# Kernel optimization log

Hardware: AMD Instinct MI355X
Metric: run time of the kernel (lower is better)

Reference implementation:

```python
import jax, jax.numpy as jnp
import numpy as np

N0, N1, N2 = 120000, 12000, 1024
E1, E2 = 300000, 10240
F_IN, H1, C1, NCLS = 602, 8, 8, 41
NEG_SLOPE = 0.2


def setup_inputs() -> dict:
    key = jax.random.key(0)
    ks = jax.random.split(key, 14)
    x = jax.random.normal(ks[0], (N0, F_IN), jnp.float32)
    edge_index1 = jnp.stack([
        jax.random.randint(ks[1], (E1,), 0, N0),
        jax.random.randint(ks[2], (E1,), 0, N1),
    ]).astype(jnp.int64)
    edge_index2 = jnp.stack([
        jax.random.randint(ks[3], (E2,), 0, N1),
        jax.random.randint(ks[4], (E2,), 0, N2),
    ]).astype(jnp.int64)
    s1 = 1.0 / np.sqrt(F_IN)
    s2 = 1.0 / np.sqrt(H1 * C1)
    W1 = jax.random.normal(ks[5], (F_IN, H1 * C1), jnp.float32) * s1
    att_src1 = jax.random.normal(ks[6], (H1, C1), jnp.float32) * s2
    att_dst1 = jax.random.normal(ks[7], (H1, C1), jnp.float32) * s2
    b1 = jnp.zeros((H1 * C1,), jnp.float32)
    W2 = jax.random.normal(ks[8], (H1 * C1, NCLS), jnp.float32) * s2
    att_src2 = jax.random.normal(ks[9], (1, NCLS), jnp.float32) * 0.1
    att_dst2 = jax.random.normal(ks[10], (1, NCLS), jnp.float32) * 0.1
    b2 = jnp.zeros((NCLS,), jnp.float32)
    return {"x": x, "edge_index1": edge_index1, "edge_index2": edge_index2,
            "size1": N1, "size2": N2,
            "W1": W1, "att_src1": att_src1, "att_dst1": att_dst1, "b1": b1,
            "W2": W2, "att_src2": att_src2, "att_dst2": att_dst2, "b2": b2}


def _seg_softmax(alpha, seg, n):
    # numerically stable softmax over edges grouped by destination node
    m = jax.lax.stop_gradient(jax.ops.segment_max(alpha, seg, num_segments=n))
    e = jnp.exp(alpha - m[seg])
    s = jax.ops.segment_sum(e, seg, num_segments=n)
    return e / (s[seg] + 1e-16)


def _gat_conv(x_src, x_dst, ei, W, a_src, a_dst, b, n_dst):
    H, C = a_src.shape
    h_src = (x_src @ W).reshape(-1, H, C)   # [N_src, H, C]
    h_dst = (x_dst @ W).reshape(-1, H, C)   # [N_dst, H, C]
    loop = jnp.arange(n_dst)
    src = jnp.concatenate([ei[0], loop])    # self-loops on dst nodes (PyG add_self_loops)
    dst = jnp.concatenate([ei[1], loop])
    a_s = (h_src * a_src).sum(-1)           # [N_src, H]
    a_d = (h_dst * a_dst).sum(-1)           # [N_dst, H]
    alpha = jax.nn.leaky_relu(a_s[src] + a_d[dst], NEG_SLOPE)  # [E, H]
    alpha = _seg_softmax(alpha, dst, n_dst)
    out = jax.ops.segment_sum(h_src[src] * alpha[:, :, None], dst, num_segments=n_dst)
    return out.reshape(n_dst, H * C) + b


def reference(x, edge_index1, edge_index2, size1, size2,
              W1, att_src1, att_dst1, b1, W2, att_src2, att_dst2, b2):
    h = _gat_conv(x, x[:size1], edge_index1, W1, att_src1, att_dst1, b1, size1)
    h = jax.nn.elu(h)
    h = _gat_conv(h, h[:size2], edge_index2, W2, att_src2, att_dst2, b2, size2)
    return jax.nn.log_softmax(h, axis=-1)
```

## Files before the change

kernel.cpp:

```cpp
#include <hip/hip_runtime.h>
#include <hip/hip_bf16.h>
#include <math.h>

typedef short bf16x8 __attribute__((ext_vector_type(8)));
typedef float f32x4 __attribute__((ext_vector_type(4)));

#define N0v 120000
#define N1v 12000
#define N2v 1024
#define F_INv 602
#define KPADv 608
#define HCv 64
#define NCLSv 41
#define NEGv 0.2f

__device__ __forceinline__ float b2f(unsigned short u) {
  return __uint_as_float(((unsigned int)u) << 16);
}
__device__ __forceinline__ unsigned short f2b(float f) {
  unsigned int u = __float_as_uint(f);
  u += 0x7fffu + ((u >> 16) & 1u);
  return (unsigned short)(u >> 16);
}
__device__ __forceinline__ unsigned int pk2(float lo, float hi) {
  __hip_bfloat162 h = __float22bfloat162_rn(make_float2(lo, hi));
  unsigned int u;
  __builtin_memcpy(&u, &h, 4);
  return u;
}
__device__ __forceinline__ float leaky(float v) {
  return v > 0.f ? v : NEGv * v;
}

__global__ void k_prep(const float* __restrict__ W1, unsigned short* __restrict__ Wt,
                       int* __restrict__ deg1, int* __restrict__ deg2) {
  int idx = blockIdx.x * 256 + threadIdx.x;
  if (idx < HCv * KPADv) {
    int n = idx / KPADv, k = idx % KPADv;
    Wt[idx] = (k < F_INv) ? f2b(W1[k * HCv + n]) : (unsigned short)0;
  }
  if (idx < N1v) deg1[idx] = 0;
  if (idx < N2v) deg2[idx] = 0;
}

__global__ __launch_bounds__(512, 4) void k_gemm1(const float* __restrict__ x,
                                                  const unsigned short* __restrict__ Wt,
                                                  unsigned short* __restrict__ H,
                                                  float* __restrict__ as1,
                                                  float* __restrict__ ad1,
                                                  const float* __restrict__ att_s,
                                                  const float* __restrict__ att_d) {
  __shared__ unsigned short Bs[64][328];
  __shared__ float sAtt[128];
  const int tid = threadIdx.x;
  const int wave = tid >> 6, lane = tid & 63;
  const int c15 = lane & 15, kseg = lane >> 4;
  const int block_row = blockIdx.x * 128;
  const int myrow = block_row + wave * 16 + c15;
  const float* rowp = x + (size_t)min(myrow, N0v - 1) * F_INv;

  if (tid < 128) sAtt[tid] = (tid < 64) ? att_s[tid] : att_d[tid - 64];

  auto stage = [&](int kofs, int nc8) {
    int chunks = 64 * nc8;
    for (int i = tid; i < chunks; i += 512) {
      int rr = i / nc8, cc = (i % nc8) * 8;
      *reinterpret_cast<uint4*>(&Bs[rr][cc]) =
          *reinterpret_cast<const uint4*>(Wt + (size_t)rr * KPADv + kofs + cc);
    }
  };

  f32x4 acc[4];
#pragma unroll
  for (int n = 0; n < 4; ++n) acc[n] = (f32x4){0.f, 0.f, 0.f, 0.f};

  float cur[8], nxt[8];
  auto loadA = [&](int kt, float (&f)[8]) {
    const int kb = kt * 32 + kseg * 8;
    const float* p = rowp + kb;
    if (kb + 8 <= F_INv) {
#pragma unroll
      for (int q = 0; q < 4; ++q) {
        float2 t = *reinterpret_cast<const float2*>(p + 2 * q);
        f[2 * q] = t.x;
        f[2 * q + 1] = t.y;
      }
    } else {
      float2 t = *reinterpret_cast<const float2*>(p);
      f[0] = t.x;
      f[1] = t.y;
#pragma unroll
      for (int q = 2; q < 8; ++q) f[q] = 0.f;
    }
  };
  auto compute = [&](int kt) {
    union {
      unsigned int u[4];
      bf16x8 v;
    } af;
#pragma unroll
    for (int q = 0; q < 4; ++q) af.u[q] = pk2(cur[2 * q], cur[2 * q + 1]);
    const int kk = (kt < 10 ? kt * 32 : kt * 32 - 320) + kseg * 8;
#pragma unroll
    for (int n = 0; n < 4; ++n) {
      bf16x8 b = *reinterpret_cast<const bf16x8*>(&Bs[n * 16 + c15][kk]);
      acc[n] = __builtin_amdgcn_mfma_f32_16x16x32_bf16(af.v, b, acc[n], 0, 0, 0);
    }
  };

  stage(0, 40);
  loadA(0, cur);
  __syncthreads();
#pragma unroll
  for (int kt = 0; kt < 10; ++kt) {
    loadA(kt + 1, nxt);
    compute(kt);
#pragma unroll
    for (int q = 0; q < 8; ++q) cur[q] = nxt[q];
  }
  __syncthreads();
  stage(320, 36);
  __syncthreads();
#pragma unroll
  for (int kt = 10; kt < 19; ++kt) {
    if (kt < 18) loadA(kt + 1, nxt);
    compute(kt);
    if (kt < 18) {
#pragma unroll
      for (int q = 0; q < 8; ++q) cur[q] = nxt[q];
    }
  }

  float attS[4], attD[4];
#pragma unroll
  for (int n = 0; n < 4; ++n) {
    attS[n] = sAtt[n * 16 + c15];
    attD[n] = sAtt[64 + n * 16 + c15];
  }
#pragma unroll
  for (int j = 0; j < 4; ++j) {
    int row = block_row + wave * 16 + kseg * 4 + j;
    bool rok = row < N0v;
#pragma unroll
    for (int n = 0; n < 4; ++n) {
      if (rok) H[(size_t)row * HCv + n * 16 + c15] = f2b(acc[n][j]);
      float ps = acc[n][j] * attS[n];
      float pd = acc[n][j] * attD[n];
      ps += __shfl_xor(ps, 1, 64);
      ps += __shfl_xor(ps, 2, 64);
      ps += __shfl_xor(ps, 4, 64);
      pd += __shfl_xor(pd, 1, 64);
      pd += __shfl_xor(pd, 2, 64);
      pd += __shfl_xor(pd, 4, 64);
      if (rok && ((c15 & 7) == 0)) {
        int hd = n * 2 + (c15 >> 3);
        as1[(size_t)row * 8 + hd] = ps;
        if (row < N1v) ad1[(size_t)row * 8 + hd] = pd;
      }
    }
  }
}

__global__ void k_count2x(const int* __restrict__ dst1, int E1, int* __restrict__ deg1,
                          const int* __restrict__ dst2, int E2, int* __restrict__ deg2) {
  int e = blockIdx.x * 256 + threadIdx.x;
  if (e < E1) atomicAdd(&deg1[dst1[e]], 1);
  if (e < E2) atomicAdd(&deg2[dst2[e]], 1);
}

template <int ELT>
__device__ __forceinline__ void scan_body(const int* __restrict__ deg, int* __restrict__ rs,
                                          int* __restrict__ cur, int n) {
  __shared__ int wsum[16];
  const int t = threadIdx.x, lane = t & 63, wid = t >> 6;
  int vals[ELT];
  int tot = 0;
#pragma unroll
  for (int e = 0; e < ELT; ++e) {
    int i = t * ELT + e;
    int v = (i < n) ? deg[i] : 0;
    vals[e] = v;
    tot += v;
  }
  int s = tot;
#pragma unroll
  for (int off = 1; off < 64; off <<= 1) {
    int u = __shfl_up(s, off, 64);
    if (lane >= off) s += u;
  }
  if (lane == 63) wsum[wid] = s;
  __syncthreads();
  if (t < 16) {
    int w = wsum[t];
#pragma unroll
    for (int off = 1; off < 16; off <<= 1) {
      int u = __shfl_up(w, off, 64);
      if (t >= off) w += u;
    }
    wsum[t] = w;
  }
  __syncthreads();
  int woff = (wid == 0) ? 0 : wsum[wid - 1];
  int run = woff + s - tot;
#pragma unroll
  for (int e = 0; e < ELT; ++e) {
    int i = t * ELT + e;
    if (i < n) {
      rs[i] = run;
      cur[i] = run;
    }
    run += vals[e];
  }
  if (t == 1023) rs[n] = run;
}

__global__ __launch_bounds__(1024) void k_scan2x(const int* __restrict__ deg1, int* __restrict__ rs1,
                                                 int* __restrict__ cur1, int n1,
                                                 const int* __restrict__ deg2, int* __restrict__ rs2,
                                                 int* __restrict__ cur2, int n2) {
  if (blockIdx.x == 0)
    scan_body<12>(deg1, rs1, cur1, n1);
  else
    scan_body<12>(deg2, rs2, cur2, n2);
}

__global__ void k_scatter2x(const int* __restrict__ src1, const int* __restrict__ dst1, int E1,
                            int* __restrict__ cur1, int* __restrict__ es1,
                            const int* __restrict__ src2, const int* __restrict__ dst2, int E2,
                            int* __restrict__ cur2, int* __restrict__ es2) {
  int e = blockIdx.x * 256 + threadIdx.x;
  if (e < E1) {
    int p = atomicAdd(&cur1[dst1[e]], 1);
    es1[p] = src1[e];
  }
  if (e < E2) {
    int p = atomicAdd(&cur2[dst2[e]], 1);
    es2[p] = src2[e];
  }
}

__global__ __launch_bounds__(256) void k_attn1f(const float* __restrict__ as1,
                                                const float* __restrict__ ad1,
                                                const int* __restrict__ rs,
                                                const int* __restrict__ esrc,
                                                const unsigned short* __restrict__ H,
                                                const float* __restrict__ b1,
                                                const float* __restrict__ W2,
                                                const float* __restrict__ avs,
                                                const float* __restrict__ avd,
                                                float* __restrict__ g,
                                                float* __restrict__ as2,
                                                float* __restrict__ ad2) {
  __shared__ float w[HCv * NCLSv];
  __shared__ float vs[NCLSv], vd[NCLSv];
  const int tid = threadIdx.x;
  for (int i = tid; i < HCv * NCLSv; i += 256) w[i] = W2[i];
  if (tid < NCLSv) {
    vs[tid] = avs[tid];
    vd[tid] = avd[tid];
  }
  __syncthreads();
  const int lane = tid & 63;
  const int d = blockIdx.x * 4 + (tid >> 6);
  if (d >= N1v) return;
  const int h = lane >> 3;
  const int beg = rs[d], end = rs[d + 1];
  const float adh = ad1[(size_t)d * 8 + h];
  const float a_self = leaky(as1[(size_t)d * 8 + h] + adh);

  float m0 = a_self, m1 = -1e30f, m2 = -1e30f, m3 = -1e30f;
  int p = beg;
  for (; p + 4 <= end; p += 4) {
    int s0 = esrc[p], s1 = esrc[p + 1], s2 = esrc[p + 2], s3 = esrc[p + 3];
    m0 = fmaxf(m0, leaky(as1[(size_t)s0 * 8 + h] + adh));
    m1 = fmaxf(m1, leaky(as1[(size_t)s1 * 8 + h] + adh));
    m2 = fmaxf(m2, leaky(as1[(size_t)s2 * 8 + h] + adh));
    m3 = fmaxf(m3, leaky(as1[(size_t)s3 * 8 + h] + adh));
  }
  for (; p < end; ++p) m1 = fmaxf(m1, leaky(as1[(size_t)esrc[p] * 8 + h] + adh));
  const float m = fmaxf(fmaxf(m0, m1), fmaxf(m2, m3));

  float ss0 = __expf(a_self - m), ss1 = 0.f, ss2 = 0.f, ss3 = 0.f;
  float ac0 = ss0 * b2f(H[(size_t)d * HCv + lane]), ac1 = 0.f, ac2 = 0.f, ac3 = 0.f;
  for (p = beg; p + 4 <= end; p += 4) {
    int s0 = esrc[p], s1 = esrc[p + 1], s2 = esrc[p + 2], s3 = esrc[p + 3];
    float e0 = __expf(leaky(as1[(size_t)s0 * 8 + h] + adh) - m);
    float e1 = __expf(leaky(as1[(size_t)s1 * 8 + h] + adh) - m);
    float e2 = __expf(leaky(as1[(size_t)s2 * 8 + h] + adh) - m);
    float e3 = __expf(leaky(as1[(size_t)s3 * 8 + h] + adh) - m);
    ac0 += e0 * b2f(H[(size_t)s0 * HCv + lane]);
    ac1 += e1 * b2f(H[(size_t)s1 * HCv + lane]);
    ac2 += e2 * b2f(H[(size_t)s2 * HCv + lane]);
    ac3 += e3 * b2f(H[(size_t)s3 * HCv + lane]);
    ss0 += e0;
    ss1 += e1;
    ss2 += e2;
    ss3 += e3;
  }
  for (; p < end; ++p) {
    int s = esrc[p];
    float e = __expf(leaky(as1[(size_t)s * 8 + h] + adh) - m);
    ss1 += e;
    ac1 += e * b2f(H[(size_t)s * HCv + lane]);
  }
  const float ssum = (ss0 + ss1) + (ss2 + ss3);
  const float acc = (ac0 + ac1) + (ac2 + ac3);
  float o = acc / ssum + b1[lane];
  o = o > 0.f ? o : expm1f(o);

  const int lc = (lane < NCLSv) ? lane : 0;
  float gc = 0.f;
#pragma unroll
  for (int k = 0; k < HCv; ++k) {
    float bc = __shfl(o, k, 64);
    gc += bc * w[k * NCLSv + lc];
  }
  if (lane < NCLSv) g[(size_t)d * NCLSv + lane] = gc;
  float sa = (lane < NCLSv) ? gc * vs[lane] : 0.f;
  float da = (lane < NCLSv) ? gc * vd[lane] : 0.f;
#pragma unroll
  for (int off = 32; off >= 1; off >>= 1) {
    sa += __shfl_xor(sa, off, 64);
    da += __shfl_xor(da, off, 64);
  }
  if (lane == 0) {
    as2[d] = sa;
    ad2[d] = da;
  }
}

__global__ __launch_bounds__(256) void k_attn2(const float* __restrict__ as2,
                                               const float* __restrict__ ad2,
                                               const int* __restrict__ rs,
                                               const int* __restrict__ esrc,
                                               const float* __restrict__ g,
                                               const float* __restrict__ b2,
                                               float* __restrict__ out) {
  int wave = threadIdx.x >> 6, lane = threadIdx.x & 63;
  int d = blockIdx.x * 4 + wave;
  if (d >= N2v) return;
  int beg = rs[d], end = rs[d + 1];
  float ad = ad2[d];
  float a_self = leaky(as2[d] + ad);
  float m = a_self;
  for (int p = beg; p < end; ++p) m = fmaxf(m, leaky(as2[esrc[p]] + ad));
  float ssum, acc;
  {
    float e = __expf(a_self - m);
    ssum = e;
    acc = (lane < NCLSv) ? e * g[(size_t)d * NCLSv + lane] : 0.f;
  }
  for (int p = beg; p < end; ++p) {
    int s = esrc[p];
    float e = __expf(leaky(as2[s] + ad) - m);
    ssum += e;
    if (lane < NCLSv) acc += e * g[(size_t)s * NCLSv + lane];
  }
  float logit = acc / ssum + ((lane < NCLSv) ? b2[lane] : 0.f);
  float v = (lane < NCLSv) ? logit : -INFINITY;
  float mx = v;
#pragma unroll
  for (int o = 32; o >= 1; o >>= 1) mx = fmaxf(mx, __shfl_xor(mx, o, 64));
  float p = (lane < NCLSv) ? __expf(v - mx) : 0.f;
  float sum = p;
#pragma unroll
  for (int o = 32; o >= 1; o >>= 1) sum += __shfl_xor(sum, o, 64);
  if (lane < NCLSv) out[(size_t)d * NCLSv + lane] = v - mx - logf(sum);
}

extern "C" void kernel_launch(void* const* d_in, const int* in_sizes, int n_in,
                              void* d_out, int out_size, void* d_ws, size_t ws_size,
                              hipStream_t stream) {
  const float* x = (const float*)d_in[0];
  const int* ei1 = (const int*)d_in[1];
  const int* ei2 = (const int*)d_in[2];
  const float* W1 = (const float*)d_in[5];
  const float* att_src1 = (const float*)d_in[6];
  const float* att_dst1 = (const float*)d_in[7];
  const float* b1 = (const float*)d_in[8];
  const float* W2 = (const float*)d_in[9];
  const float* att_src2 = (const float*)d_in[10];
  const float* att_dst2 = (const float*)d_in[11];
  const float* b2 = (const float*)d_in[12];
  float* out = (float*)d_out;

  const int E1 = in_sizes[1] / 2;
  const int E2 = in_sizes[2] / 2;
  const int* src1 = ei1;
  const int* dst1 = ei1 + E1;
  const int* src2 = ei2;
  const int* dst2 = ei2 + E2;

  char* w = (char*)d_ws;
  size_t off = 0;
  auto alloc = [&](size_t bytes) {
    void* p = w + off;
    off += (bytes + 255) & ~(size_t)255;
    return p;
  };
  unsigned short* Wt  = (unsigned short*)alloc((size_t)HCv * KPADv * 2);
  unsigned short* H   = (unsigned short*)alloc((size_t)N0v * HCv * 2);
  float* as1 = (float*)alloc((size_t)N0v * 8 * 4);
  float* ad1 = (float*)alloc((size_t)N1v * 8 * 4);
  int* deg1  = (int*)alloc((size_t)N1v * 4);
  int* rs1   = (int*)alloc((size_t)(N1v + 1) * 4);
  int* cur1  = (int*)alloc((size_t)N1v * 4);
  int* es1   = (int*)alloc((size_t)E1 * 4);
  float* g   = (float*)alloc((size_t)N1v * NCLSv * 4);
  float* as2 = (float*)alloc((size_t)N1v * 4);
  float* ad2 = (float*)alloc((size_t)N1v * 4);
  int* deg2  = (int*)alloc((size_t)N2v * 4);
  int* rs2   = (int*)alloc((size_t)(N2v + 1) * 4);
  int* cur2  = (int*)alloc((size_t)N2v * 4);
  int* es2   = (int*)alloc((size_t)E2 * 4);
  (void)ws_size; (void)n_in; (void)out_size;

  k_prep<<<(HCv * KPADv + 255) / 256, 256, 0, stream>>>(W1, Wt, deg1, deg2);
  k_gemm1<<<(N0v + 127) / 128, 512, 0, stream>>>(x, Wt, H, as1, ad1, att_src1, att_dst1);

  k_count2x<<<(E1 + 255) / 256, 256, 0, stream>>>(dst1, E1, deg1, dst2, E2, deg2);
  k_scan2x<<<2, 1024, 0, stream>>>(deg1, rs1, cur1, N1v, deg2, rs2, cur2, N2v);
  k_scatter2x<<<(E1 + 255) / 256, 256, 0, stream>>>(src1, dst1, E1, cur1, es1,
                                                    src2, dst2, E2, cur2, es2);
  k_attn1f<<<(N1v + 3) / 4, 256, 0, stream>>>(as1, ad1, rs1, es1, H, b1,
                                              W2, att_src2, att_dst2, g, as2, ad2);
  k_attn2<<<N2v / 4, 256, 0, stream>>>(as2, ad2, rs2, es2, g, b2, out);
}
```

Baseline: 186.4 us.

## Fuse degree count into GEMM and merge graph tail into a cooperative kernel

Result: slower. 455.4 us (+144.3%).

```diff
diff --git a/kernel.cpp b/kernel.cpp
--- a/kernel.cpp
+++ b/kernel.cpp
@@ -1,6 +1,9 @@
 #include <hip/hip_runtime.h>
 #include <hip/hip_bf16.h>
+#include <hip/hip_cooperative_groups.h>
 #include <math.h>
+
+namespace cg = cooperative_groups;
 
 typedef short bf16x8 __attribute__((ext_vector_type(8)));
 typedef float f32x4 __attribute__((ext_vector_type(4)));
@@ -49,7 +52,11 @@
                                                   float* __restrict__ as1,
                                                   float* __restrict__ ad1,
                                                   const float* __restrict__ att_s,
-                                                  const float* __restrict__ att_d) {
+                                                  const float* __restrict__ att_d,
+                                                  const int* __restrict__ dst1, int E1,
+                                                  int* __restrict__ deg1,
+                                                  const int* __restrict__ dst2, int E2,
+                                                  int* __restrict__ deg2) {
   __shared__ unsigned short Bs[64][328];
   __shared__ float sAtt[128];
   const int tid = threadIdx.x;
@@ -110,6 +117,11 @@
 
   stage(0, 40);
   loadA(0, cur);
+  {
+    int e = blockIdx.x * 512 + tid;
+    if (e < E1) atomicAdd(&deg1[dst1[e]], 1);
+    if (e < E2) atomicAdd(&deg2[dst2[e]], 1);
+  }
   __syncthreads();
 #pragma unroll
   for (int kt = 0; kt < 10; ++kt) {
@@ -161,67 +173,195 @@
   }
 }
 
-__global__ void k_count2x(const int* __restrict__ dst1, int E1, int* __restrict__ deg1,
-                          const int* __restrict__ dst2, int E2, int* __restrict__ deg2) {
-  int e = blockIdx.x * 256 + threadIdx.x;
-  if (e < E1) atomicAdd(&deg1[dst1[e]], 1);
-  if (e < E2) atomicAdd(&deg2[dst2[e]], 1);
-}
-
-template <int ELT>
-__device__ __forceinline__ void scan_body(const int* __restrict__ deg, int* __restrict__ rs,
-                                          int* __restrict__ cur, int n) {
-  __shared__ int wsum[16];
+__device__ void scan_seq(const int* __restrict__ deg, int* __restrict__ rs,
+                         int* __restrict__ cur, int n) {
+  __shared__ int ws[4];
   const int t = threadIdx.x, lane = t & 63, wid = t >> 6;
-  int vals[ELT];
+  const int chunk = (n + 255) >> 8;
+  const int lo = t * chunk, hi = min(n, lo + chunk);
   int tot = 0;
-#pragma unroll
-  for (int e = 0; e < ELT; ++e) {
-    int i = t * ELT + e;
-    int v = (i < n) ? deg[i] : 0;
-    vals[e] = v;
-    tot += v;
-  }
+  for (int i = lo; i < hi; ++i) tot += deg[i];
   int s = tot;
 #pragma unroll
   for (int off = 1; off < 64; off <<= 1) {
     int u = __shfl_up(s, off, 64);
     if (lane >= off) s += u;
   }
-  if (lane == 63) wsum[wid] = s;
+  if (lane == 63) ws[wid] = s;
   __syncthreads();
-  if (t < 16) {
-    int w = wsum[t];
-#pragma unroll
-    for (int off = 1; off < 16; off <<= 1) {
-      int u = __shfl_up(w, off, 64);
-      if (t >= off) w += u;
-    }
-    wsum[t] = w;
-  }
-  __syncthreads();
-  int woff = (wid == 0) ? 0 : wsum[wid - 1];
+  int woff = 0;
+#pragma unroll
+  for (int j = 0; j < 3; ++j)
+    if (wid > j) woff += ws[j];
   int run = woff + s - tot;
-#pragma unroll
-  for (int e = 0; e < ELT; ++e) {
-    int i = t * ELT + e;
-    if (i < n) {
-      rs[i] = run;
-      cur[i] = run;
-    }
-    run += vals[e];
-  }
-  if (t == 1023) rs[n] = run;
-}
-
-__global__ __launch_bounds__(1024) void k_scan2x(const int* __restrict__ deg1, int* __restrict__ rs1,
-                                                 int* __restrict__ cur1, int n1,
-                                                 const int* __restrict__ deg2, int* __restrict__ rs2,
-                                                 int* __restrict__ cur2, int n2) {
+  for (int i = lo; i < hi; ++i) {
+    rs[i] = run;
+    cur[i] = run;
+    run += deg[i];
+  }
+  if (t == 255) rs[n] = run;
+}
+
+__device__ __forceinline__ void attn1_body(int d, int lane, const int* rs1, const int* es1,
+                                           const float* as1, const float* ad1,
+                                           const unsigned short* H, const float* b1,
+                                           const float* w, const float* vs, const float* vd,
+                                           float* g, float* as2, float* ad2) {
+  const int h = lane >> 3;
+  const int lc = (lane < NCLSv) ? lane : 0;
+  const int beg = rs1[d], end = rs1[d + 1];
+  const float adh = ad1[(size_t)d * 8 + h];
+  const float a_self = leaky(as1[(size_t)d * 8 + h] + adh);
+
+  float m0 = a_self, m1 = -1e30f, m2 = -1e30f, m3 = -1e30f;
+  int p = beg;
+  for (; p + 4 <= end; p += 4) {
+    int s0 = es1[p], s1 = es1[p + 1], s2 = es1[p + 2], s3 = es1[p + 3];
+    m0 = fmaxf(m0, leaky(as1[(size_t)s0 * 8 + h] + adh));
+    m1 = fmaxf(m1, leaky(as1[(size_t)s1 * 8 + h] + adh));
+    m2 = fmaxf(m2, leaky(as1[(size_t)s2 * 8 + h] + adh));
+    m3 = fmaxf(m3, leaky(as1[(size_t)s3 * 8 + h] + adh));
+  }
+  for (; p < end; ++p) m1 = fmaxf(m1, leaky(as1[(size_t)es1[p] * 8 + h] + adh));
+  const float m = fmaxf(fmaxf(m0, m1), fmaxf(m2, m3));
+
+  float ss0 = __expf(a_self - m), ss1 = 0.f, ss2 = 0.f, ss3 = 0.f;
+  float ac0 = ss0 * b2f(H[(size_t)d * HCv + lane]), ac1 = 0.f, ac2 = 0.f, ac3 = 0.f;
+  for (p = beg; p + 4 <= end; p += 4) {
+    int s0 = es1[p], s1 = es1[p + 1], s2 = es1[p + 2], s3 = es1[p + 3];
+    float e0 = __expf(leaky(as1[(size_t)s0 * 8 + h] + adh) - m);
+    float e1 = __expf(leaky(as1[(size_t)s1 * 8 + h] + adh) - m);
+    float e2 = __expf(leaky(as1[(size_t)s2 * 8 + h] + adh) - m);
+    float e3 = __expf(leaky(as1[(size_t)s3 * 8 + h] + adh) - m);
+    ac0 += e0 * b2f(H[(size_t)s0 * HCv + lane]);
+    ac1 += e1 * b2f(H[(size_t)s1 * HCv + lane]);
+    ac2 += e2 * b2f(H[(size_t)s2 * HCv + lane]);
+    ac3 += e3 * b2f(H[(size_t)s3 * HCv + lane]);
+    ss0 += e0;
+    ss1 += e1;
+    ss2 += e2;
+    ss3 += e3;
+  }
+  for (; p < end; ++p) {
+    int s = es1[p];
+    float e = __expf(leaky(as1[(size_t)s * 8 + h] + adh) - m);
+    ss1 += e;
+    ac1 += e * b2f(H[(size_t)s * HCv + lane]);
+  }
+  const float ssum = (ss0 + ss1) + (ss2 + ss3);
+  const float acc = (ac0 + ac1) + (ac2 + ac3);
+  float o = acc / ssum + b1[lane];
+  o = o > 0.f ? o : expm1f(o);
+
+  float gc = 0.f;
+#pragma unroll
+  for (int k = 0; k < HCv; ++k) {
+    float bc = __shfl(o, k, 64);
+    gc += bc * w[k * NCLSv + lc];
+  }
+  if (lane < NCLSv) g[(size_t)d * NCLSv + lane] = gc;
+  float sa = (lane < NCLSv) ? gc * vs[lane] : 0.f;
+  float da = (lane < NCLSv) ? gc * vd[lane] : 0.f;
+#pragma unroll
+  for (int off = 32; off >= 1; off >>= 1) {
+    sa += __shfl_xor(sa, off, 64);
+    da += __shfl_xor(da, off, 64);
+  }
+  if (lane == 0) {
+    as2[d] = sa;
+    ad2[d] = da;
+  }
+}
+
+__device__ __forceinline__ void attn2_body(int d, int lane, const int* rs2, const int* es2,
+                                           const float* as2, const float* ad2, const float* g,
+                                           const float* b2, float* out) {
+  int beg = rs2[d], end = rs2[d + 1];
+  float ad = ad2[d];
+  float a_self = leaky(as2[d] + ad);
+  float m = a_self;
+  for (int p = beg; p < end; ++p) m = fmaxf(m, leaky(as2[es2[p]] + ad));
+  float ssum, acc;
+  {
+    float e = __expf(a_self - m);
+    ssum = e;
+    acc = (lane < NCLSv) ? e * g[(size_t)d * NCLSv + lane] : 0.f;
+  }
+  for (int p = beg; p < end; ++p) {
+    int s = es2[p];
+    float e = __expf(leaky(as2[s] + ad) - m);
+    ssum += e;
+    if (lane < NCLSv) acc += e * g[(size_t)s * NCLSv + lane];
+  }
+  float logit = acc / ssum + ((lane < NCLSv) ? b2[lane] : 0.f);
+  float v = (lane < NCLSv) ? logit : -INFINITY;
+  float mx = v;
+#pragma unroll
+  for (int off = 32; off >= 1; off >>= 1) mx = fmaxf(mx, __shfl_xor(mx, off, 64));
+  float p = (lane < NCLSv) ? __expf(v - mx) : 0.f;
+  float sum = p;
+#pragma unroll
+  for (int off = 32; off >= 1; off >>= 1) sum += __shfl_xor(sum, off, 64);
+  if (lane < NCLSv) out[(size_t)d * NCLSv + lane] = v - mx - logf(sum);
+}
+
+__global__ __launch_bounds__(256, 4) void k_tail(
+    const int* __restrict__ src1, const int* __restrict__ dst1, int E1,
+    const int* __restrict__ deg1, int* __restrict__ rs1, int* __restrict__ cur1,
+    int* __restrict__ es1,
+    const int* __restrict__ src2, const int* __restrict__ dst2, int E2,
+    const int* __restrict__ deg2, int* __restrict__ rs2, int* __restrict__ cur2,
+    int* __restrict__ es2,
+    const float* __restrict__ as1, const float* __restrict__ ad1,
+    const unsigned short* __restrict__ H, const float* __restrict__ b1,
+    const float* __restrict__ W2, const float* __restrict__ avs, const float* __restrict__ avd,
+    float* __restrict__ g, float* __restrict__ as2, float* __restrict__ ad2,
+    const float* __restrict__ b2, float* __restrict__ out) {
+  cg::grid_group grid = cg::this_grid();
+  __shared__ float w[HCv * NCLSv];
+  __shared__ float vs[NCLSv], vd[NCLSv];
+  const int tid = threadIdx.x;
+  const int gid = blockIdx.x * 256 + tid;
+  const int gsz = gridDim.x * 256;
+  const int lane = tid & 63;
+  const int gwave = blockIdx.x * 4 + (tid >> 6);
+  const int nwv = gridDim.x * 4;
+
+  for (int i = tid; i < HCv * NCLSv; i += 256) w[i] = W2[i];
+  if (tid < NCLSv) {
+    vs[tid] = avs[tid];
+    vd[tid] = avd[tid];
+  }
+
   if (blockIdx.x == 0)
-    scan_body<12>(deg1, rs1, cur1, n1);
+    scan_seq(deg1, rs1, cur1, N1v);
+  else if (blockIdx.x == 1)
+    scan_seq(deg2, rs2, cur2, N2v);
+  grid.sync();
+  for (int e = gid; e < E1; e += gsz) {
+    int p = atomicAdd(&cur1[dst1[e]], 1);
+    es1[p] = src1[e];
+  }
+  for (int e = gid; e < E2; e += gsz) {
+    int p = atomicAdd(&cur2[dst2[e]], 1);
+    es2[p] = src2[e];
+  }
+  grid.sync();
+  for (int d = gwave; d < N1v; d += nwv)
+    attn1_body(d, lane, rs1, es1, as1, ad1, H, b1, w, vs, vd, g, as2, ad2);
+  grid.sync();
+  for (int d = gwave; d < N2v; d += nwv)
+    attn2_body(d, lane, rs2, es2, as2, ad2, g, b2, out);
+}
+
+__global__ __launch_bounds__(256) void k_scan2x(const int* __restrict__ deg1, int* __restrict__ rs1,
+                                                int* __restrict__ cur1,
+                                                const int* __restrict__ deg2, int* __restrict__ rs2,
+                                                int* __restrict__ cur2) {
+  if (blockIdx.x == 0)
+    scan_seq(deg1, rs1, cur1, N1v);
   else
-    scan_body<12>(deg2, rs2, cur2, n2);
+    scan_seq(deg2, rs2, cur2, N2v);
 }
 
 __global__ void k_scatter2x(const int* __restrict__ src1, const int* __restrict__ dst1, int E1,
@@ -260,73 +400,9 @@
     vd[tid] = avd[tid];
   }
   __syncthreads();
-  const int lane = tid & 63;
   const int d = blockIdx.x * 4 + (tid >> 6);
   if (d >= N1v) return;
-  const int h = lane >> 3;
-  const int beg = rs[d], end = rs[d + 1];
-  const float adh = ad1[(size_t)d * 8 + h];
-  const float a_self = leaky(as1[(size_t)d * 8 + h] + adh);
-
-  float m0 = a_self, m1 = -1e30f, m2 = -1e30f, m3 = -1e30f;
-  int p = beg;
-  for (; p + 4 <= end; p += 4) {
-    int s0 = esrc[p], s1 = esrc[p + 1], s2 = esrc[p + 2], s3 = esrc[p + 3];
-    m0 = fmaxf(m0, leaky(as1[(size_t)s0 * 8 + h] + adh));
-    m1 = fmaxf(m1, leaky(as1[(size_t)s1 * 8 + h] + adh));
-    m2 = fmaxf(m2, leaky(as1[(size_t)s2 * 8 + h] + adh));
-    m3 = fmaxf(m3, leaky(as1[(size_t)s3 * 8 + h] + adh));
-  }
-  for (; p < end; ++p) m1 = fmaxf(m1, leaky(as1[(size_t)esrc[p] * 8 + h] + adh));
-  const float m = fmaxf(fmaxf(m0, m1), fmaxf(m2, m3));
-
-  float ss0 = __expf(a_self - m), ss1 = 0.f, ss2 = 0.f, ss3 = 0.f;
-  float ac0 = ss0 * b2f(H[(size_t)d * HCv + lane]), ac1 = 0.f, ac2 = 0.f, ac3 = 0.f;
-  for (p = beg; p + 4 <= end; p += 4) {
-    int s0 = esrc[p], s1 = esrc[p + 1], s2 = esrc[p + 2], s3 = esrc[p + 3];
-    float e0 = __expf(leaky(as1[(size_t)s0 * 8 + h] + adh) - m);
-    float e1 = __expf(leaky(as1[(size_t)s1 * 8 + h] + adh) - m);
-    float e2 = __expf(leaky(as1[(size_t)s2 * 8 + h] + adh) - m);
-    float e3 = __expf(leaky(as1[(size_t)s3 * 8 + h] + adh) - m);
-    ac0 += e0 * b2f(H[(size_t)s0 * HCv + lane]);
-    ac1 += e1 * b2f(H[(size_t)s1 * HCv + lane]);
-    ac2 += e2 * b2f(H[(size_t)s2 * HCv + lane]);
-    ac3 += e3 * b2f(H[(size_t)s3 * HCv + lane]);
-    ss0 += e0;
-    ss1 += e1;
-    ss2 += e2;
-    ss3 += e3;
-  }
-  for (; p < end; ++p) {
-    int s = esrc[p];
-    float e = __expf(leaky(as1[(size_t)s * 8 + h] + adh) - m);
-    ss1 += e;
-    ac1 += e * b2f(H[(size_t)s * HCv + lane]);
-  }
-  const float ssum = (ss0 + ss1) + (ss2 + ss3);
-  const float acc = (ac0 + ac1) + (ac2 + ac3);
-  float o = acc / ssum + b1[lane];
-  o = o > 0.f ? o : expm1f(o);
-
-  const int lc = (lane < NCLSv) ? lane : 0;
-  float gc = 0.f;
-#pragma unroll
-  for (int k = 0; k < HCv; ++k) {
-    float bc = __shfl(o, k, 64);
-    gc += bc * w[k * NCLSv + lc];
-  }
-  if (lane < NCLSv) g[(size_t)d * NCLSv + lane] = gc;
-  float sa = (lane < NCLSv) ? gc * vs[lane] : 0.f;
-  float da = (lane < NCLSv) ? gc * vd[lane] : 0.f;
-#pragma unroll
-  for (int off = 32; off >= 1; off >>= 1) {
-    sa += __shfl_xor(sa, off, 64);
-    da += __shfl_xor(da, off, 64);
-  }
-  if (lane == 0) {
-    as2[d] = sa;
-    ad2[d] = da;
-  }
+  attn1_body(d, tid & 63, rs, esrc, as1, ad1, H, b1, w, vs, vd, g, as2, ad2);
 }
 
 __global__ __launch_bounds__(256) void k_attn2(const float* __restrict__ as2,
@@ -336,36 +412,9 @@
                                                const float* __restrict__ g,
                                                const float* __restrict__ b2,
                                                float* __restrict__ out) {
-  int wave = threadIdx.x >> 6, lane = threadIdx.x & 63;
-  int d = blockIdx.x * 4 + wave;
+  int d = blockIdx.x * 4 + (threadIdx.x >> 6);
   if (d >= N2v) return;
-  int beg = rs[d], end = rs[d + 1];
-  float ad = ad2[d];
-  float a_self = leaky(as2[d] + ad);
-  float m = a_self;
-  for (int p = beg; p < end; ++p) m = fmaxf(m, leaky(as2[esrc[p]] + ad));
-  float ssum, acc;
-  {
-    float e = __expf(a_self - m);
-    ssum = e;
-    acc = (lane < NCLSv) ? e * g[(size_t)d * NCLSv + lane] : 0.f;
-  }
-  for (int p = beg; p < end; ++p) {
-    int s = esrc[p];
-    float e = __expf(leaky(as2[s] + ad) - m);
-    ssum += e;
-    if (lane < NCLSv) acc += e * g[(size_t)s * NCLSv + lane];
-  }
-  float logit = acc / ssum + ((lane < NCLSv) ? b2[lane] : 0.f);
-  float v = (lane < NCLSv) ? logit : -INFINITY;
-  float mx = v;
-#pragma unroll
-  for (int o = 32; o >= 1; o >>= 1) mx = fmaxf(mx, __shfl_xor(mx, o, 64));
-  float p = (lane < NCLSv) ? __expf(v - mx) : 0.f;
-  float sum = p;
-#pragma unroll
-  for (int o = 32; o >= 1; o >>= 1) sum += __shfl_xor(sum, o, 64);
-  if (lane < NCLSv) out[(size_t)d * NCLSv + lane] = v - mx - logf(sum);
+  attn2_body(d, threadIdx.x & 63, rs, esrc, as2, ad2, g, b2, out);
 }
 
 extern "C" void kernel_launch(void* const* d_in, const int* in_sizes, int n_in,
@@ -382,10 +431,10 @@
   const float* att_src2 = (const float*)d_in[10];
   const float* att_dst2 = (const float*)d_in[11];
   const float* b2 = (const float*)d_in[12];
-  float* out = (float*)d_out;
-
-  const int E1 = in_sizes[1] / 2;
-  const int E2 = in_sizes[2] / 2;
+  float* outp = (float*)d_out;
+
+  int E1 = in_sizes[1] / 2;
+  int E2 = in_sizes[2] / 2;
   const int* src1 = ei1;
   const int* dst1 = ei1 + E1;
   const int* src2 = ei2;
@@ -416,13 +465,40 @@
   (void)ws_size; (void)n_in; (void)out_size;
 
   k_prep<<<(HCv * KPADv + 255) / 256, 256, 0, stream>>>(W1, Wt, deg1, deg2);
-  k_gemm1<<<(N0v + 127) / 128, 512, 0, stream>>>(x, Wt, H, as1, ad1, att_src1, att_dst1);
-
-  k_count2x<<<(E1 + 255) / 256, 256, 0, stream>>>(dst1, E1, deg1, dst2, E2, deg2);
-  k_scan2x<<<2, 1024, 0, stream>>>(deg1, rs1, cur1, N1v, deg2, rs2, cur2, N2v);
-  k_scatter2x<<<(E1 + 255) / 256, 256, 0, stream>>>(src1, dst1, E1, cur1, es1,
-                                                    src2, dst2, E2, cur2, es2);
-  k_attn1f<<<(N1v + 3) / 4, 256, 0, stream>>>(as1, ad1, rs1, es1, H, b1,
-                                              W2, att_src2, att_dst2, g, as2, ad2);
-  k_attn2<<<N2v / 4, 256, 0, stream>>>(as2, ad2, rs2, es2, g, b2, out);
-}
+  k_gemm1<<<(N0v + 127) / 128, 512, 0, stream>>>(x, Wt, H, as1, ad1, att_src1, att_dst1,
+                                                 dst1, E1, deg1, dst2, E2, deg2);
+
+  bool coop_done = false;
+  {
+    int dev = 0;
+    if (hipGetDevice(&dev) == hipSuccess) {
+      int numCU = 0, blocksPerCU = 0;
+      if (hipDeviceGetAttribute(&numCU, hipDeviceAttributeMultiprocessorCount, dev) == hipSuccess &&
+          hipOccupancyMaxActiveBlocksPerMultiprocessor(&blocksPerCU, k_tail, 256, 0) == hipSuccess &&
+          numCU > 0 && blocksPerCU > 0) {
+        int gridsz = blocksPerCU * numCU;
+        if (gridsz >= 2) {
+          void* args[] = {
+              (void*)&src1, (void*)&dst1, (void*)&E1,
+              (void*)&deg1, (void*)&rs1, (void*)&cur1, (void*)&es1,
+              (void*)&src2, (void*)&dst2, (void*)&E2,
+              (void*)&deg2, (void*)&rs2, (void*)&cur2, (void*)&es2,
+              (void*)&as1, (void*)&ad1, (void*)&H, (void*)&b1,
+              (void*)&W2, (void*)&att_src2, (void*)&att_dst2,
+              (void*)&g, (void*)&as2, (void*)&ad2, (void*)&b2, (void*)&outp};
+          if (hipLaunchCooperativeKernel((const void*)k_tail, dim3(gridsz), dim3(256), args, 0,
+                                         stream) == hipSuccess)
+            coop_done = true;
+        }
+      }
+    }
+  }
+  if (!coop_done) {
+    k_scan2x<<<2, 256, 0, stream>>>(deg1, rs1, cur1, deg2, rs2, cur2);
+    k_scatter2x<<<(E1 + 255) / 256, 256, 0, stream>>>(src1, dst1, E1, cur1, es1,
+                                                      src2, dst2, E2, cur2, es2);
+    k_attn1f<<<(N1v + 3) / 4, 256, 0, stream>>>(as1, ad1, rs1, es1, H, b1,
+                                                W2, att_src2, att_dst2, g, as2, ad2);
+    k_attn2<<<N2v / 4, 256, 0, stream>>>(as2, ad2, rs2, es2, g, b2, outp);
+  }
+}
```

## Fuse degree counting into GEMM kernel and deepen A-operand prefetch

Applied to the files above, without the earlier changes.

Measured after the change: 179.3 us, median of 2. 1.04x faster.

```diff
diff --git a/kernel.cpp b/kernel.cpp
--- a/kernel.cpp
+++ b/kernel.cpp
@@ -49,7 +49,11 @@
                                                   float* __restrict__ as1,
                                                   float* __restrict__ ad1,
                                                   const float* __restrict__ att_s,
-                                                  const float* __restrict__ att_d) {
+                                                  const float* __restrict__ att_d,
+                                                  const int* __restrict__ dst1, int E1,
+                                                  int* __restrict__ deg1,
+                                                  const int* __restrict__ dst2, int E2,
+                                                  int* __restrict__ deg2) {
   __shared__ unsigned short Bs[64][328];
   __shared__ float sAtt[128];
   const int tid = threadIdx.x;
@@ -74,7 +78,10 @@
 #pragma unroll
   for (int n = 0; n < 4; ++n) acc[n] = (f32x4){0.f, 0.f, 0.f, 0.f};
 
-  float cur[8], nxt[8];
+  float tA[8], tB[8], tC[8];
+  auto bufref = [&](int i) -> float(&)[8] {
+    return (i % 3 == 0) ? tA : ((i % 3 == 1) ? tB : tC);
+  };
   auto loadA = [&](int kt, float (&f)[8]) {
     const int kb = kt * 32 + kseg * 8;
     const float* p = rowp + kb;
@@ -93,13 +100,13 @@
       for (int q = 2; q < 8; ++q) f[q] = 0.f;
     }
   };
-  auto compute = [&](int kt) {
+  auto compute = [&](int kt, const float (&f)[8]) {
     union {
       unsigned int u[4];
       bf16x8 v;
     } af;
 #pragma unroll
-    for (int q = 0; q < 4; ++q) af.u[q] = pk2(cur[2 * q], cur[2 * q + 1]);
+    for (int q = 0; q < 4; ++q) af.u[q] = pk2(f[2 * q], f[2 * q + 1]);
     const int kk = (kt < 10 ? kt * 32 : kt * 32 - 320) + kseg * 8;
 #pragma unroll
     for (int n = 0; n < 4; ++n) {
@@ -109,26 +116,26 @@
   };
 
   stage(0, 40);
-  loadA(0, cur);
+  loadA(0, tA);
+  loadA(1, tB);
+  {
+    int e = blockIdx.x * 512 + tid;
+    if (e < E1) atomicAdd(&deg1[dst1[e]], 1);
+    if (e < E2) atomicAdd(&deg2[dst2[e]], 1);
+  }
   __syncthreads();
 #pragma unroll
   for (int kt = 0; kt < 10; ++kt) {
-    loadA(kt + 1, nxt);
-    compute(kt);
-#pragma unroll
-    for (int q = 0; q < 8; ++q) cur[q] = nxt[q];
+    if (kt + 2 < 19) loadA(kt + 2, bufref(kt + 2));
+    compute(kt, bufref(kt));
   }
   __syncthreads();
   stage(320, 36);
   __syncthreads();
 #pragma unroll
   for (int kt = 10; kt < 19; ++kt) {
-    if (kt < 18) loadA(kt + 1, nxt);
-    compute(kt);
-    if (kt < 18) {
-#pragma unroll
-      for (int q = 0; q < 8; ++q) cur[q] = nxt[q];
-    }
+    if (kt + 2 < 19) loadA(kt + 2, bufref(kt + 2));
+    compute(kt, bufref(kt));
   }
 
   float attS[4], attD[4];
@@ -159,13 +166,6 @@
       }
     }
   }
-}
-
-__global__ void k_count2x(const int* __restrict__ dst1, int E1, int* __restrict__ deg1,
-                          const int* __restrict__ dst2, int E2, int* __restrict__ deg2) {
-  int e = blockIdx.x * 256 + threadIdx.x;
-  if (e < E1) atomicAdd(&deg1[dst1[e]], 1);
-  if (e < E2) atomicAdd(&deg2[dst2[e]], 1);
 }
 
 template <int ELT>
@@ -416,9 +416,8 @@
   (void)ws_size; (void)n_in; (void)out_size;
 
   k_prep<<<(HCv * KPADv + 255) / 256, 256, 0, stream>>>(W1, Wt, deg1, deg2);
-  k_gemm1<<<(N0v + 127) / 128, 512, 0, stream>>>(x, Wt, H, as1, ad1, att_src1, att_dst1);
-
-  k_count2x<<<(E1 + 255) / 256, 256, 0, stream>>>(dst1, E1, deg1, dst2, E2, deg2);
+  k_gemm1<<<(N0v + 127) / 128, 512, 0, stream>>>(x, Wt, H, as1, ad1, att_src1, att_dst1,
+                                                 dst1, E1, deg1, dst2, E2, deg2);
   k_scan2x<<<2, 1024, 0, stream>>>(deg1, rs1, cur1, N1v, deg2, rs2, cur2, N2v);
   k_scatter2x<<<(E1 + 255) / 256, 256, 0, stream>>>(src1, dst1, E1, cur1, es1,
                                                     src2, dst2, E2, cur2, es2);
```
